# Performance work log

Measured on AMD Instinct MI355X. Metric: run time of the kernel, lower is better.

## Reference

```python
import jax, jax.numpy as jnp
import numpy as np

B, S, D, H = 4, 2048, 512, 8
DEPTH = D // H
BAND = 16  # log_thresholds [1,2,4,8,16] union == distance <= 16


def setup_inputs() -> dict:
    key = jax.random.key(0)
    ks = jax.random.split(key, 11)
    sc = 0.02
    return {
        "q": jax.random.normal(ks[0], (B, S, D), jnp.float32),
        "k": jax.random.normal(ks[1], (B, S, D), jnp.float32),
        "v": jax.random.normal(ks[2], (B, S, D), jnp.float32),
        "wq": jax.random.normal(ks[3], (D, D), jnp.float32) * sc,
        "bq": jnp.zeros((D,), jnp.float32),
        "wk": jax.random.normal(ks[4], (D, D), jnp.float32) * sc,
        "bk": jnp.zeros((D,), jnp.float32),
        "wv": jax.random.normal(ks[5], (D, D), jnp.float32) * sc,
        "bv": jnp.zeros((D,), jnp.float32),
        "wo": jax.random.normal(ks[6], (D, D), jnp.float32) * sc,
        "bo": jnp.zeros((D,), jnp.float32),
    }


def _split_heads(x):
    # [B,S,D] -> [B,H,S,depth]
    b, s, _ = x.shape
    return x.reshape(b, s, H, DEPTH).transpose(0, 2, 1, 3)


def reference(q, k, v, wq, bq, wk, bk, wv, bv, wo, bo):
    qh = _split_heads(q @ wq + bq)
    kh = _split_heads(k @ wk + bk)
    vh = _split_heads(v @ wv + bv)
    scale = 1.0 / jnp.sqrt(jnp.float32(DEPTH))
    logits = jnp.einsum("bhqd,bhkd->bhqk", qh, kh) * scale  # [B,H,S,S]
    idx = jnp.arange(S)
    keep = jnp.abs(idx[:, None] - idx[None, :]) <= BAND  # band mask [S,S]
    logits = jnp.where(keep[None, None], logits, jnp.float32(-1e9))
    attn = jax.nn.softmax(logits, axis=-1)
    out = jnp.einsum("bhqk,bhkd->bhqd", attn, vh)
    out = out.transpose(0, 2, 1, 3).reshape(q.shape[0], -1, D)
    return out @ wo + bo
```

## Files before the change

### kernel.cpp

```cpp
#include <hip/hip_runtime.h>

typedef unsigned int uint;
typedef unsigned short ushort;
typedef __attribute__((ext_vector_type(8))) short bf16x8;
typedef __attribute__((ext_vector_type(4))) float f32x4;

namespace {
constexpr int kS = 2048;
constexpr int kD = 512;
constexpr int kH = 8;
constexpr int kBand = 16;

template <bool C, typename A, typename B> struct cond { using type = A; };
template <typename A, typename B> struct cond<false, A, B> { using type = B; };
}

static __device__ __forceinline__ ushort f2bf(float f) {
  uint u = __builtin_bit_cast(uint, f);
  u = (u + 0x7fffu + ((u >> 16) & 1u)) >> 16;
  return (ushort)u;
}

static __device__ __forceinline__ bf16x8 cvt8(f32x4 lo, f32x4 hi) {
  uint4 r;
  asm("v_cvt_pk_bf16_f32 %0, %1, %2" : "=v"(r.x) : "v"(lo[0]), "v"(lo[1]));
  asm("v_cvt_pk_bf16_f32 %0, %1, %2" : "=v"(r.y) : "v"(lo[2]), "v"(lo[3]));
  asm("v_cvt_pk_bf16_f32 %0, %1, %2" : "=v"(r.z) : "v"(hi[0]), "v"(hi[1]));
  asm("v_cvt_pk_bf16_f32 %0, %1, %2" : "=v"(r.w) : "v"(hi[2]), "v"(hi[3]));
  return __builtin_bit_cast(bf16x8, r);
}

#define GLD16(gp, lp)                                                   \
  __builtin_amdgcn_global_load_lds(                                     \
      (const __attribute__((address_space(1))) uint*)(gp),              \
      (__attribute__((address_space(3))) uint*)(lp), 16, 0, 0)

__global__ __launch_bounds__(256) void prep_kernel(
    const float* __restrict__ wq, const float* __restrict__ wk,
    const float* __restrict__ wv, const float* __restrict__ wo,
    ushort* __restrict__ WT) {
  __shared__ float Ws[64][65];
  const int w = blockIdx.x;
  const int tid = threadIdx.x;
  const int z = w >> 6;
  const float* W = z == 0 ? wq : (z == 1 ? wk : (z == 2 ? wv : wo));
  ushort* T = WT + (size_t)z * kD * kD;
  const int kt = ((w >> 3) & 7) * 64, nt = (w & 7) * 64;
  const int r = tid >> 2, c0 = (tid & 3) * 16;
#pragma unroll
  for (int i = 0; i < 4; ++i) {
    const float4 x =
        *(const float4*)(W + (size_t)(kt + r) * kD + nt + c0 + i * 4);
    Ws[r][c0 + i * 4 + 0] = x.x;
    Ws[r][c0 + i * 4 + 1] = x.y;
    Ws[r][c0 + i * 4 + 2] = x.z;
    Ws[r][c0 + i * 4 + 3] = x.w;
  }
  __syncthreads();
  const int n = tid >> 2, k0 = (tid & 3) * 16;
  alignas(16) ushort tmp[16];
#pragma unroll
  for (int i = 0; i < 16; ++i) tmp[i] = f2bf(Ws[k0 + i][n]);
  ushort* dst = T + (size_t)(nt + n) * kD + kt + k0;
  *(uint4*)(dst + 0) = *(const uint4*)&tmp[0];
  *(uint4*)(dst + 8) = *(const uint4*)&tmp[8];
}

template <int TM, bool AF32>
__global__ __launch_bounds__(256) void gemm_kernel(
    const float* __restrict__ qf, const float* __restrict__ kf,
    const float* __restrict__ vf, const ushort* __restrict__ obp,
    const ushort* __restrict__ WT, const float* __restrict__ bq,
    const float* __restrict__ bk, const float* __restrict__ bv,
    const float* __restrict__ bo, ushort* __restrict__ Qp,
    ushort* __restrict__ Kp, ushort* __restrict__ VT,
    float* __restrict__ outp, int mode_arg) {
  const int mode = mode_arg + blockIdx.z;
  const void* Abv;
  const float* bias;
  switch (mode) {
    case 0: Abv = qf; bias = bq; break;
    case 1: Abv = kf; bias = bk; break;
    case 2: Abv = vf; bias = bv; break;
    default: Abv = obp; bias = bo; break;
  }
  using AT = typename cond<AF32, float, ushort>::type;
  const AT* Abt = (const AT*)Abv;
  const ushort* BT = WT + (size_t)mode * kD * kD;

  constexpr int A_STAGE = TM * (AF32 ? 64 : 32);
  constexpr int B_BASE = 3 * A_STAGE;
  constexpr int NI = (TM == 128) ? 4 : 2;
  constexpr int AI = AF32 ? TM / 32 : TM / 64;
  __shared__ alignas(16) ushort smem[B_BASE + 12288];

  const int tid = threadIdx.x;
  const int wave = tid >> 6, lane = tid & 63, l15 = lane & 15, qd = lane >> 4;
  const int wm = (TM == 128) ? (wave >> 1) * 64 : 0;
  const int wn = (TM == 128) ? (wave & 1) * 64 : wave * 32;
  const int lin = blockIdx.x;
  const int xcd = lin & 7, j = lin >> 3;
  const int rblk = xcd + 8 * (j >> 2), cblk = j & 3;
  const int row0 = rblk * TM, col0 = cblk * 128;
  const int sw = (l15 & 3) ^ (l15 >> 2);

  const AT* pA[AI];
  const ushort* pB[2];
  uint ldsA[AI], ldsB[2];
#pragma unroll
  for (int i = 0; i < AI; ++i) {
    const int linear = i * 256 + tid;
    int r, g;
    if constexpr (AF32) {
      r = linear >> 3;
      g = (linear & 7) ^ (r & 7);
    } else {
      r = linear >> 2;
      g = (linear & 3) ^ ((r & 3) ^ ((r >> 2) & 3));
    }
    pA[i] = Abt + (size_t)(row0 + r) * kD + g * (AF32 ? 4 : 8);
    ldsA[i] = (uint)(i * 256 + wave * 64) * 8;
  }
#pragma unroll
  for (int i = 0; i < 2; ++i) {
    const int linear = i * 256 + tid;
    const int r = linear >> 2, c = linear & 3;
    const int g = c ^ ((r & 3) ^ ((r >> 2) & 3));
    pB[i] = BT + (size_t)(col0 + r) * kD + g * 8;
    ldsB[i] = (uint)B_BASE + (uint)(i * 256 + wave * 64) * 8;
  }

#define ISSUE(kk, st)                                                     \
  {                                                                       \
    _Pragma("unroll") for (int i = 0; i < AI; ++i)                        \
        GLD16(pA[i] + (kk), &smem[ldsA[i] + (st) * A_STAGE]);             \
    _Pragma("unroll") for (int i = 0; i < 2; ++i)                         \
        GLD16(pB[i] + (kk), &smem[ldsB[i] + (st) * 4096]);                \
  }

  f32x4 acc[4][NI];
#pragma unroll
  for (int mi = 0; mi < 4; ++mi)
#pragma unroll
    for (int ni = 0; ni < NI; ++ni) acc[mi][ni] = (f32x4)(0.f);

  ISSUE(0, 0);
  ISSUE(32, 1);
#pragma unroll
  for (int it = 0; it < 16; ++it) {
    if (it < 15) {
      if constexpr (AI + 2 == 6) {
        asm volatile("s_waitcnt vmcnt(6) lgkmcnt(0)\n\ts_barrier" ::: "memory");
      } else {
        static_assert(AI + 2 == 3 || AI + 2 == 6, "unexpected stage size");
        asm volatile("s_waitcnt vmcnt(3) lgkmcnt(0)\n\ts_barrier" ::: "memory");
      }
    } else {
      asm volatile("s_waitcnt vmcnt(0) lgkmcnt(0)\n\ts_barrier" ::: "memory");
    }
    if (it < 14) ISSUE((it + 2) * 32, (it + 2) % 3);
    bf16x8 af[4], br[NI];
    if constexpr (AF32) {
      const float* as = (const float*)&smem[(it % 3) * A_STAGE];
#pragma unroll
      for (int mi = 0; mi < 4; ++mi) {
        const int row = wm + mi * 16 + l15;
        const int s2 = l15 & 7;
        const f32x4 lo = *(const f32x4*)&as[row * 32 + ((2 * qd) ^ s2) * 4];
        const f32x4 hi = *(const f32x4*)&as[row * 32 + ((2 * qd + 1) ^ s2) * 4];
        af[mi] = cvt8(lo, hi);
      }
    } else {
      const ushort* as = &smem[(it % 3) * A_STAGE];
#pragma unroll
      for (int mi = 0; mi < 4; ++mi)
        af[mi] = *(const bf16x8*)&as[(wm + mi * 16 + l15) * 32 + (qd ^ sw) * 8];
    }
    const ushort* bs = &smem[B_BASE + (it % 3) * 4096];
#pragma unroll
    for (int ni = 0; ni < NI; ++ni)
      br[ni] = *(const bf16x8*)&bs[(wn + ni * 16 + l15) * 32 + (qd ^ sw) * 8];
#pragma unroll
    for (int mi = 0; mi < 4; ++mi)
#pragma unroll
      for (int ni = 0; ni < NI; ++ni)
        acc[mi][ni] = __builtin_amdgcn_mfma_f32_16x16x32_bf16(
            af[mi], br[ni], acc[mi][ni], 0, 0, 0);
  }
#undef ISSUE

  float bcol[NI];
#pragma unroll
  for (int ni = 0; ni < NI; ++ni) bcol[ni] = bias[col0 + wn + ni * 16 + l15];

  if (mode == 3) {
#pragma unroll
    for (int mi = 0; mi < 4; ++mi)
#pragma unroll
      for (int ni = 0; ni < NI; ++ni) {
        const int n_g = col0 + wn + ni * 16 + l15;
#pragma unroll
        for (int r = 0; r < 4; ++r) {
          const int token = row0 + wm + mi * 16 + qd * 4 + r;
          outp[(size_t)token * kD + n_g] = acc[mi][ni][r] + bcol[ni];
        }
      }
    return;
  }

  __syncthreads();

  ushort* T = &smem[wave * 4608];
  if (mode <= 1) {
#pragma unroll
    for (int mi = 0; mi < 4; ++mi)
#pragma unroll
      for (int ni = 0; ni < NI; ++ni)
#pragma unroll
        for (int r = 0; r < 4; ++r)
          T[(mi * 16 + qd * 4 + r) * 72 + ni * 16 + l15] =
              f2bf(acc[mi][ni][r] + bcol[ni]);
  } else {
#pragma unroll
    for (int mi = 0; mi < 4; ++mi)
#pragma unroll
      for (int ni = 0; ni < NI; ++ni)
#pragma unroll
        for (int r = 0; r < 4; ++r)
          T[(ni * 16 + l15) * 72 + mi * 16 + qd * 4 + r] =
              f2bf(acc[mi][ni][r] + bcol[ni]);
  }
  asm volatile("s_waitcnt lgkmcnt(0)" ::: "memory");

  const ushort* Trow = &smem[wave * 4608 + lane * 72];
  if (mode <= 1) {
    ushort* C = (mode == 0) ? Qp : Kp;
    ushort* dst = C + (size_t)(row0 + wm + lane) * kD + col0 + wn;
#pragma unroll
    for (int c = 0; c < 8; ++c)
      *(uint4*)(dst + c * 8) = *(const uint4*)(Trow + c * 8);
  } else {
    const int n_g = col0 + wn + lane;
    const int h = n_g >> 6, d = n_g & 63;
    const int t0 = row0 + wm;
    const int b = t0 >> 11, ss = t0 & (kS - 1);
    ushort* dst = VT + ((size_t)(b * kH + h) * 64 + d) * kS + ss;
#pragma unroll
    for (int c = 0; c < 8; ++c)
      *(uint4*)(dst + c * 8) = *(const uint4*)(Trow + c * 8);
  }
}

__global__ __launch_bounds__(64, 1) void attn_kernel(
    const ushort* __restrict__ Qp, const ushort* __restrict__ Kp,
    const ushort* __restrict__ VT, ushort* __restrict__ Ob) {
  __shared__ alignas(16) ushort Pl[64 * 104];

  const int lane = threadIdx.x, l15 = lane & 15, qd = lane >> 4;
  const int bh = blockIdx.y, b = bh >> 3, h = bh & 7;
  const int q0 = blockIdx.x * 64;
  const int colA = h * 64;

  bf16x8 qf[4][2], kf[6][2];
#pragma unroll
  for (int mi = 0; mi < 4; ++mi) {
    const size_t base =
        ((size_t)b * kS + q0 + mi * 16 + l15) * kD + colA + qd * 8;
#pragma unroll
    for (int kc = 0; kc < 2; ++kc)
      qf[mi][kc] = *(const bf16x8*)&Qp[base + kc * 32];
  }
#pragma unroll
  for (int ni = 0; ni < 6; ++ni) {
    int key = q0 - kBand + ni * 16 + l15;
    key = key < 0 ? 0 : (key > kS - 1 ? kS - 1 : key);
    const size_t base = ((size_t)b * kS + key) * kD + colA + qd * 8;
#pragma unroll
    for (int kc = 0; kc < 2; ++kc)
      kf[ni][kc] = *(const bf16x8*)&Kp[base + kc * 32];
  }

  f32x4 S[4][6];
#pragma unroll
  for (int mi = 0; mi < 4; ++mi)
#pragma unroll
    for (int ni = 0; ni < 6; ++ni) S[mi][ni] = (f32x4)(0.f);
#pragma unroll
  for (int mi = 0; mi < 4; ++mi)
#pragma unroll
    for (int ni = 0; ni < 6; ++ni)
#pragma unroll
      for (int kc = 0; kc < 2; ++kc)
        S[mi][ni] = __builtin_amdgcn_mfma_f32_16x16x32_bf16(
            qf[mi][kc], kf[ni][kc], S[mi][ni], 0, 0, 0);

#pragma unroll
  for (int mi = 0; mi < 4; ++mi)
#pragma unroll
    for (int ni = 0; ni < 6; ++ni)
#pragma unroll
      for (int r = 0; r < 4; ++r) {
        const int q_local = mi * 16 + qd * 4 + r;
        const int key_local = ni * 16 + l15;
        const int key = q0 - kBand + key_local;
        const int dlt = key_local - q_local;
        const bool ok = (dlt >= 0) && (dlt <= 32) && (key >= 0) && (key < kS);
        S[mi][ni][r] = ok ? S[mi][ni][r] * 0.125f : -3.0e38f;
      }

  float inv[4][4];
#pragma unroll
  for (int mi = 0; mi < 4; ++mi)
#pragma unroll
    for (int r = 0; r < 4; ++r) {
      float m = S[mi][0][r];
#pragma unroll
      for (int ni = 1; ni < 6; ++ni) m = fmaxf(m, S[mi][ni][r]);
      m = fmaxf(m, __shfl_xor(m, 1));
      m = fmaxf(m, __shfl_xor(m, 2));
      m = fmaxf(m, __shfl_xor(m, 4));
      m = fmaxf(m, __shfl_xor(m, 8));
      float s = 0.f;
#pragma unroll
      for (int ni = 0; ni < 6; ++ni) {
        const float e = __expf(S[mi][ni][r] - m);
        S[mi][ni][r] = e;
        s += e;
      }
      s += __shfl_xor(s, 1);
      s += __shfl_xor(s, 2);
      s += __shfl_xor(s, 4);
      s += __shfl_xor(s, 8);
      inv[mi][r] = 1.f / s;
    }

#pragma unroll
  for (int mi = 0; mi < 4; ++mi)
#pragma unroll
    for (int ni = 0; ni < 6; ++ni)
#pragma unroll
      for (int r = 0; r < 4; ++r)
        Pl[(mi * 16 + qd * 4 + r) * 104 + ni * 16 + l15] = f2bf(S[mi][ni][r]);
  __syncthreads();

  f32x4 O[4][4];
#pragma unroll
  for (int mi = 0; mi < 4; ++mi)
#pragma unroll
    for (int nt = 0; nt < 4; ++nt) O[mi][nt] = (f32x4)(0.f);

#pragma unroll
  for (int kc = 0; kc < 3; ++kc) {
    bf16x8 pf[4], vfr[4];
#pragma unroll
    for (int mi = 0; mi < 4; ++mi)
      pf[mi] = *(const bf16x8*)&Pl[(mi * 16 + l15) * 104 + kc * 32 + qd * 8];
    int kb0 = q0 - kBand + kc * 32 + qd * 8;
    kb0 = kb0 < 0 ? 0 : (kb0 > kS - 8 ? kS - 8 : kb0);
#pragma unroll
    for (int nt = 0; nt < 4; ++nt)
      vfr[nt] =
          *(const bf16x8*)&VT[((size_t)bh * 64 + nt * 16 + l15) * kS + kb0];
#pragma unroll
    for (int mi = 0; mi < 4; ++mi)
#pragma unroll
      for (int nt = 0; nt < 4; ++nt)
        O[mi][nt] = __builtin_amdgcn_mfma_f32_16x16x32_bf16(pf[mi], vfr[nt],
                                                            O[mi][nt], 0, 0, 0);
  }

#pragma unroll
  for (int mi = 0; mi < 4; ++mi)
#pragma unroll
    for (int nt = 0; nt < 4; ++nt)
#pragma unroll
      for (int r = 0; r < 4; ++r)
        Pl[(mi * 16 + qd * 4 + r) * 72 + nt * 16 + l15] =
            f2bf(O[mi][nt][r] * inv[mi][r]);
  asm volatile("s_waitcnt lgkmcnt(0)" ::: "memory");

  ushort* dst = Ob + ((size_t)b * kS + q0 + lane) * kD + colA;
  const ushort* Trow = &Pl[lane * 72];
#pragma unroll
  for (int c = 0; c < 8; ++c)
    *(uint4*)(dst + c * 8) = *(const uint4*)(Trow + c * 8);
}

extern "C" void kernel_launch(void* const* d_in, const int* in_sizes, int n_in,
                              void* d_out, int out_size, void* d_ws,
                              size_t ws_size, hipStream_t stream) {
  const float* q = (const float*)d_in[0];
  const float* k = (const float*)d_in[1];
  const float* v = (const float*)d_in[2];
  const float* wq = (const float*)d_in[3];
  const float* bq = (const float*)d_in[4];
  const float* wk = (const float*)d_in[5];
  const float* bk = (const float*)d_in[6];
  const float* wv = (const float*)d_in[7];
  const float* bv = (const float*)d_in[8];
  const float* wo = (const float*)d_in[9];
  const float* bo = (const float*)d_in[10];
  float* out = (float*)d_out;

  const size_t n1 = (size_t)8192 * kD;
  ushort* Qp = (ushort*)d_ws;
  ushort* Kp = Qp + n1;
  ushort* VT = Kp + n1;
  ushort* Ob = VT + n1;
  ushort* WT = Ob + n1;

  prep_kernel<<<dim3(256), 256, 0, stream>>>(wq, wk, wv, wo, WT);
  gemm_kernel<128, true><<<dim3(256, 1, 3), 256, 0, stream>>>(
      q, k, v, Ob, WT, bq, bk, bv, bo, Qp, Kp, VT, out, 0);
  attn_kernel<<<dim3(kS / 64, 32), 64, 0, stream>>>(Qp, Kp, VT, Ob);
  gemm_kernel<64, false><<<dim3(512, 1, 1), 256, 0, stream>>>(
      q, k, v, Ob, WT, bq, bk, bv, bo, Qp, Kp, VT, out, 3);
}
```

Baseline: 163.7 us.

## Convert fp32 A to bf16 on load in QKV GEMM, shrink attention tiles

The QKV projection GEMM now loads fp32 activations into registers, converts them to bf16 and writes them to LDS one stage ahead, instead of staging raw fp32 via global_load_lds. This halves A-tile LDS footprint and LDS read traffic and allows three blocks per CU, at the cost of register-staged loads. The attention kernel now processes 32 queries per block instead of 64, with a smaller key window and two blocks per CU, for more parallelism and less wasted band compute. The output projection becomes its own specialized kernel.

Result: no change. 161.6 us (-1.3%).

```diff
diff --git a/kernel.cpp b/kernel.cpp
--- a/kernel.cpp
+++ b/kernel.cpp
@@ -10,9 +10,6 @@
 constexpr int kD = 512;
 constexpr int kH = 8;
 constexpr int kBand = 16;
-
-template <bool C, typename A, typename B> struct cond { using type = A; };
-template <typename A, typename B> struct cond<false, A, B> { using type = B; };
 }
 
 static __device__ __forceinline__ ushort f2bf(float f) {
@@ -34,6 +31,8 @@
   __builtin_amdgcn_global_load_lds(                                     \
       (const __attribute__((address_space(1))) uint*)(gp),              \
       (__attribute__((address_space(3))) uint*)(lp), 16, 0, 0)
+
+#define FENCE asm volatile("" ::: "memory")
 
 __global__ __launch_bounds__(256) void prep_kernel(
     const float* __restrict__ wq, const float* __restrict__ wk,
@@ -66,61 +65,39 @@
   *(uint4*)(dst + 8) = *(const uint4*)&tmp[8];
 }
 
-template <int TM, bool AF32>
-__global__ __launch_bounds__(256) void gemm_kernel(
-    const float* __restrict__ qf, const float* __restrict__ kf,
-    const float* __restrict__ vf, const ushort* __restrict__ obp,
-    const ushort* __restrict__ WT, const float* __restrict__ bq,
-    const float* __restrict__ bk, const float* __restrict__ bv,
-    const float* __restrict__ bo, ushort* __restrict__ Qp,
-    ushort* __restrict__ Kp, ushort* __restrict__ VT,
-    float* __restrict__ outp, int mode_arg) {
-  const int mode = mode_arg + blockIdx.z;
-  const void* Abv;
-  const float* bias;
-  switch (mode) {
-    case 0: Abv = qf; bias = bq; break;
-    case 1: Abv = kf; bias = bk; break;
-    case 2: Abv = vf; bias = bv; break;
-    default: Abv = obp; bias = bo; break;
-  }
-  using AT = typename cond<AF32, float, ushort>::type;
-  const AT* Abt = (const AT*)Abv;
+__global__ __launch_bounds__(256, 3) void gemm_qkv(
+    const float* __restrict__ q, const float* __restrict__ k,
+    const float* __restrict__ v, const ushort* __restrict__ WT,
+    const float* __restrict__ bq, const float* __restrict__ bk,
+    const float* __restrict__ bv, ushort* __restrict__ Qp,
+    ushort* __restrict__ Kp, ushort* __restrict__ VT) {
+  const int mode = blockIdx.z;
+  const float* Ab = mode == 0 ? q : (mode == 1 ? k : v);
+  const float* bias = mode == 0 ? bq : (mode == 1 ? bk : bv);
   const ushort* BT = WT + (size_t)mode * kD * kD;
 
-  constexpr int A_STAGE = TM * (AF32 ? 64 : 32);
+  constexpr int A_STAGE = 128 * 32;
   constexpr int B_BASE = 3 * A_STAGE;
-  constexpr int NI = (TM == 128) ? 4 : 2;
-  constexpr int AI = AF32 ? TM / 32 : TM / 64;
   __shared__ alignas(16) ushort smem[B_BASE + 12288];
 
   const int tid = threadIdx.x;
   const int wave = tid >> 6, lane = tid & 63, l15 = lane & 15, qd = lane >> 4;
-  const int wm = (TM == 128) ? (wave >> 1) * 64 : 0;
-  const int wn = (TM == 128) ? (wave & 1) * 64 : wave * 32;
+  const int wm = (wave >> 1) * 64, wn = (wave & 1) * 64;
   const int lin = blockIdx.x;
   const int xcd = lin & 7, j = lin >> 3;
   const int rblk = xcd + 8 * (j >> 2), cblk = j & 3;
-  const int row0 = rblk * TM, col0 = cblk * 128;
+  const int row0 = rblk * 128, col0 = cblk * 128;
   const int sw = (l15 & 3) ^ (l15 >> 2);
 
-  const AT* pA[AI];
+  const int ar = tid >> 1;
+  const int acp = (tid & 1) * 2;
+  const int as_ = (ar & 3) ^ ((ar >> 2) & 3);
+  const float* pAg = Ab + (size_t)(row0 + ar) * kD + acp * 8;
+  const uint wA0 = (uint)(ar * 32 + ((acp ^ as_) * 8));
+  const uint wA1 = (uint)(ar * 32 + (((acp + 1) ^ as_) * 8));
+
   const ushort* pB[2];
-  uint ldsA[AI], ldsB[2];
-#pragma unroll
-  for (int i = 0; i < AI; ++i) {
-    const int linear = i * 256 + tid;
-    int r, g;
-    if constexpr (AF32) {
-      r = linear >> 3;
-      g = (linear & 7) ^ (r & 7);
-    } else {
-      r = linear >> 2;
-      g = (linear & 3) ^ ((r & 3) ^ ((r >> 2) & 3));
-    }
-    pA[i] = Abt + (size_t)(row0 + r) * kD + g * (AF32 ? 4 : 8);
-    ldsA[i] = (uint)(i * 256 + wave * 64) * 8;
-  }
+  uint ldsB[2];
 #pragma unroll
   for (int i = 0; i < 2; ++i) {
     const int linear = i * 256 + tid;
@@ -130,83 +107,71 @@
     ldsB[i] = (uint)B_BASE + (uint)(i * 256 + wave * 64) * 8;
   }
 
-#define ISSUE(kk, st)                                                     \
-  {                                                                       \
-    _Pragma("unroll") for (int i = 0; i < AI; ++i)                        \
-        GLD16(pA[i] + (kk), &smem[ldsA[i] + (st) * A_STAGE]);             \
-    _Pragma("unroll") for (int i = 0; i < 2; ++i)                         \
-        GLD16(pB[i] + (kk), &smem[ldsB[i] + (st) * 4096]);                \
-  }
-
-  f32x4 acc[4][NI];
+  f32x4 areg[2][4];
+#define LOADA(slot, kk)                                               \
+  { _Pragma("unroll") for (int c = 0; c < 4; ++c)                     \
+      areg[slot][c] = *(const f32x4*)(pAg + (kk) + c * 4); }
+#define WRITEA(st, slot)                                              \
+  {                                                                   \
+    *(bf16x8*)&smem[(st) * A_STAGE + wA0] =                           \
+        cvt8(areg[slot][0], areg[slot][1]);                           \
+    *(bf16x8*)&smem[(st) * A_STAGE + wA1] =                           \
+        cvt8(areg[slot][2], areg[slot][3]);                           \
+  }
+#define ISSUEB(kk, st)                                                \
+  { _Pragma("unroll") for (int i = 0; i < 2; ++i)                     \
+      GLD16(pB[i] + (kk), &smem[ldsB[i] + (st) * 4096]); }
+
+  f32x4 acc[4][4];
 #pragma unroll
   for (int mi = 0; mi < 4; ++mi)
 #pragma unroll
-    for (int ni = 0; ni < NI; ++ni) acc[mi][ni] = (f32x4)(0.f);
-
-  ISSUE(0, 0);
-  ISSUE(32, 1);
+    for (int ni = 0; ni < 4; ++ni) acc[mi][ni] = (f32x4)(0.f);
+
+  LOADA(0, 0);
+  FENCE;
+  ISSUEB(0, 0);
+  FENCE;
+  LOADA(1, 32);
+  FENCE;
+  ISSUEB(32, 1);
+  FENCE;
+  WRITEA(0, 0);
+
 #pragma unroll
   for (int it = 0; it < 16; ++it) {
     if (it < 15) {
-      if constexpr (AI + 2 == 6) {
-        asm volatile("s_waitcnt vmcnt(6) lgkmcnt(0)\n\ts_barrier" ::: "memory");
-      } else {
-        static_assert(AI + 2 == 3 || AI + 2 == 6, "unexpected stage size");
-        asm volatile("s_waitcnt vmcnt(3) lgkmcnt(0)\n\ts_barrier" ::: "memory");
-      }
+      WRITEA((it + 1) % 3, (it + 1) & 1);
+      if (it < 14) LOADA(it & 1, (it + 2) * 32);
+      asm volatile("s_waitcnt lgkmcnt(0)\n\ts_barrier" ::: "memory");
+      if (it < 14) ISSUEB((it + 2) * 32, (it + 2) % 3);
+      FENCE;
     } else {
       asm volatile("s_waitcnt vmcnt(0) lgkmcnt(0)\n\ts_barrier" ::: "memory");
     }
-    if (it < 14) ISSUE((it + 2) * 32, (it + 2) % 3);
-    bf16x8 af[4], br[NI];
-    if constexpr (AF32) {
-      const float* as = (const float*)&smem[(it % 3) * A_STAGE];
-#pragma unroll
-      for (int mi = 0; mi < 4; ++mi) {
-        const int row = wm + mi * 16 + l15;
-        const int s2 = l15 & 7;
-        const f32x4 lo = *(const f32x4*)&as[row * 32 + ((2 * qd) ^ s2) * 4];
-        const f32x4 hi = *(const f32x4*)&as[row * 32 + ((2 * qd + 1) ^ s2) * 4];
-        af[mi] = cvt8(lo, hi);
-      }
-    } else {
-      const ushort* as = &smem[(it % 3) * A_STAGE];
-#pragma unroll
-      for (int mi = 0; mi < 4; ++mi)
-        af[mi] = *(const bf16x8*)&as[(wm + mi * 16 + l15) * 32 + (qd ^ sw) * 8];
-    }
+    const ushort* as2 = &smem[(it % 3) * A_STAGE];
     const ushort* bs = &smem[B_BASE + (it % 3) * 4096];
-#pragma unroll
-    for (int ni = 0; ni < NI; ++ni)
+    bf16x8 af[4], br[4];
+#pragma unroll
+    for (int mi = 0; mi < 4; ++mi)
+      af[mi] = *(const bf16x8*)&as2[(wm + mi * 16 + l15) * 32 + (qd ^ sw) * 8];
+#pragma unroll
+    for (int ni = 0; ni < 4; ++ni)
       br[ni] = *(const bf16x8*)&bs[(wn + ni * 16 + l15) * 32 + (qd ^ sw) * 8];
 #pragma unroll
     for (int mi = 0; mi < 4; ++mi)
 #pragma unroll
-      for (int ni = 0; ni < NI; ++ni)
+      for (int ni = 0; ni < 4; ++ni)
         acc[mi][ni] = __builtin_amdgcn_mfma_f32_16x16x32_bf16(
             af[mi], br[ni], acc[mi][ni], 0, 0, 0);
   }
-#undef ISSUE
-
-  float bcol[NI];
-#pragma unroll
-  for (int ni = 0; ni < NI; ++ni) bcol[ni] = bias[col0 + wn + ni * 16 + l15];
-
-  if (mode == 3) {
-#pragma unroll
-    for (int mi = 0; mi < 4; ++mi)
-#pragma unroll
-      for (int ni = 0; ni < NI; ++ni) {
-        const int n_g = col0 + wn + ni * 16 + l15;
-#pragma unroll
-        for (int r = 0; r < 4; ++r) {
-          const int token = row0 + wm + mi * 16 + qd * 4 + r;
-          outp[(size_t)token * kD + n_g] = acc[mi][ni][r] + bcol[ni];
-        }
-      }
-    return;
-  }
+#undef LOADA
+#undef WRITEA
+#undef ISSUEB
+
+  float bcol[4];
+#pragma unroll
+  for (int ni = 0; ni < 4; ++ni) bcol[ni] = bias[col0 + wn + ni * 16 + l15];
 
   __syncthreads();
 
@@ -215,7 +180,7 @@
 #pragma unroll
     for (int mi = 0; mi < 4; ++mi)
 #pragma unroll
-      for (int ni = 0; ni < NI; ++ni)
+      for (int ni = 0; ni < 4; ++ni)
 #pragma unroll
         for (int r = 0; r < 4; ++r)
           T[(mi * 16 + qd * 4 + r) * 72 + ni * 16 + l15] =
@@ -224,7 +189,7 @@
 #pragma unroll
     for (int mi = 0; mi < 4; ++mi)
 #pragma unroll
-      for (int ni = 0; ni < NI; ++ni)
+      for (int ni = 0; ni < 4; ++ni)
 #pragma unroll
         for (int r = 0; r < 4; ++r)
           T[(ni * 16 + l15) * 72 + mi * 16 + qd * 4 + r] =
@@ -251,19 +216,19 @@
   }
 }
 
-__global__ __launch_bounds__(64, 1) void attn_kernel(
+__global__ __launch_bounds__(64, 2) void attn_kernel(
     const ushort* __restrict__ Qp, const ushort* __restrict__ Kp,
     const ushort* __restrict__ VT, ushort* __restrict__ Ob) {
-  __shared__ alignas(16) ushort Pl[64 * 104];
+  __shared__ alignas(16) ushort Pl[32 * 72];
 
   const int lane = threadIdx.x, l15 = lane & 15, qd = lane >> 4;
   const int bh = blockIdx.y, b = bh >> 3, h = bh & 7;
-  const int q0 = blockIdx.x * 64;
+  const int q0 = blockIdx.x * 32;
   const int colA = h * 64;
 
-  bf16x8 qf[4][2], kf[6][2];
-#pragma unroll
-  for (int mi = 0; mi < 4; ++mi) {
+  bf16x8 qf[2][2], kf[4][2];
+#pragma unroll
+  for (int mi = 0; mi < 2; ++mi) {
     const size_t base =
         ((size_t)b * kS + q0 + mi * 16 + l15) * kD + colA + qd * 8;
 #pragma unroll
@@ -271,7 +236,7 @@
       qf[mi][kc] = *(const bf16x8*)&Qp[base + kc * 32];
   }
 #pragma unroll
-  for (int ni = 0; ni < 6; ++ni) {
+  for (int ni = 0; ni < 4; ++ni) {
     int key = q0 - kBand + ni * 16 + l15;
     key = key < 0 ? 0 : (key > kS - 1 ? kS - 1 : key);
     const size_t base = ((size_t)b * kS + key) * kD + colA + qd * 8;
@@ -280,24 +245,24 @@
       kf[ni][kc] = *(const bf16x8*)&Kp[base + kc * 32];
   }
 
-  f32x4 S[4][6];
-#pragma unroll
-  for (int mi = 0; mi < 4; ++mi)
-#pragma unroll
-    for (int ni = 0; ni < 6; ++ni) S[mi][ni] = (f32x4)(0.f);
-#pragma unroll
-  for (int mi = 0; mi < 4; ++mi)
-#pragma unroll
-    for (int ni = 0; ni < 6; ++ni)
+  f32x4 S[2][4];
+#pragma unroll
+  for (int mi = 0; mi < 2; ++mi)
+#pragma unroll
+    for (int ni = 0; ni < 4; ++ni) S[mi][ni] = (f32x4)(0.f);
+#pragma unroll
+  for (int mi = 0; mi < 2; ++mi)
+#pragma unroll
+    for (int ni = 0; ni < 4; ++ni)
 #pragma unroll
       for (int kc = 0; kc < 2; ++kc)
         S[mi][ni] = __builtin_amdgcn_mfma_f32_16x16x32_bf16(
             qf[mi][kc], kf[ni][kc], S[mi][ni], 0, 0, 0);
 
 #pragma unroll
-  for (int mi = 0; mi < 4; ++mi)
-#pragma unroll
-    for (int ni = 0; ni < 6; ++ni)
+  for (int mi = 0; mi < 2; ++mi)
+#pragma unroll
+    for (int ni = 0; ni < 4; ++ni)
 #pragma unroll
       for (int r = 0; r < 4; ++r) {
         const int q_local = mi * 16 + qd * 4 + r;
@@ -308,21 +273,21 @@
         S[mi][ni][r] = ok ? S[mi][ni][r] * 0.125f : -3.0e38f;
       }
 
-  float inv[4][4];
-#pragma unroll
-  for (int mi = 0; mi < 4; ++mi)
+  float inv[2][4];
+#pragma unroll
+  for (int mi = 0; mi < 2; ++mi)
 #pragma unroll
     for (int r = 0; r < 4; ++r) {
       float m = S[mi][0][r];
 #pragma unroll
-      for (int ni = 1; ni < 6; ++ni) m = fmaxf(m, S[mi][ni][r]);
+      for (int ni = 1; ni < 4; ++ni) m = fmaxf(m, S[mi][ni][r]);
       m = fmaxf(m, __shfl_xor(m, 1));
       m = fmaxf(m, __shfl_xor(m, 2));
       m = fmaxf(m, __shfl_xor(m, 4));
       m = fmaxf(m, __shfl_xor(m, 8));
       float s = 0.f;
 #pragma unroll
-      for (int ni = 0; ni < 6; ++ni) {
+      for (int ni = 0; ni < 4; ++ni) {
         const float e = __expf(S[mi][ni][r] - m);
         S[mi][ni][r] = e;
         s += e;
@@ -335,26 +300,26 @@
     }
 
 #pragma unroll
-  for (int mi = 0; mi < 4; ++mi)
-#pragma unroll
-    for (int ni = 0; ni < 6; ++ni)
+  for (int mi = 0; mi < 2; ++mi)
+#pragma unroll
+    for (int ni = 0; ni < 4; ++ni)
 #pragma unroll
       for (int r = 0; r < 4; ++r)
-        Pl[(mi * 16 + qd * 4 + r) * 104 + ni * 16 + l15] = f2bf(S[mi][ni][r]);
+        Pl[(mi * 16 + qd * 4 + r) * 72 + ni * 16 + l15] = f2bf(S[mi][ni][r]);
   __syncthreads();
 
-  f32x4 O[4][4];
-#pragma unroll
-  for (int mi = 0; mi < 4; ++mi)
+  f32x4 O[2][4];
+#pragma unroll
+  for (int mi = 0; mi < 2; ++mi)
 #pragma unroll
     for (int nt = 0; nt < 4; ++nt) O[mi][nt] = (f32x4)(0.f);
 
 #pragma unroll
-  for (int kc = 0; kc < 3; ++kc) {
-    bf16x8 pf[4], vfr[4];
-#pragma unroll
-    for (int mi = 0; mi < 4; ++mi)
-      pf[mi] = *(const bf16x8*)&Pl[(mi * 16 + l15) * 104 + kc * 32 + qd * 8];
+  for (int kc = 0; kc < 2; ++kc) {
+    bf16x8 pf[2], vfr[4];
+#pragma unroll
+    for (int mi = 0; mi < 2; ++mi)
+      pf[mi] = *(const bf16x8*)&Pl[(mi * 16 + l15) * 72 + kc * 32 + qd * 8];
     int kb0 = q0 - kBand + kc * 32 + qd * 8;
     kb0 = kb0 < 0 ? 0 : (kb0 > kS - 8 ? kS - 8 : kb0);
 #pragma unroll
@@ -362,7 +327,7 @@
       vfr[nt] =
           *(const bf16x8*)&VT[((size_t)bh * 64 + nt * 16 + l15) * kS + kb0];
 #pragma unroll
-    for (int mi = 0; mi < 4; ++mi)
+    for (int mi = 0; mi < 2; ++mi)
 #pragma unroll
       for (int nt = 0; nt < 4; ++nt)
         O[mi][nt] = __builtin_amdgcn_mfma_f32_16x16x32_bf16(pf[mi], vfr[nt],
@@ -370,7 +335,7 @@
   }
 
 #pragma unroll
-  for (int mi = 0; mi < 4; ++mi)
+  for (int mi = 0; mi < 2; ++mi)
 #pragma unroll
     for (int nt = 0; nt < 4; ++nt)
 #pragma unroll
@@ -379,11 +344,101 @@
             f2bf(O[mi][nt][r] * inv[mi][r]);
   asm volatile("s_waitcnt lgkmcnt(0)" ::: "memory");
 
-  ushort* dst = Ob + ((size_t)b * kS + q0 + lane) * kD + colA;
-  const ushort* Trow = &Pl[lane * 72];
-#pragma unroll
-  for (int c = 0; c < 8; ++c)
+  const int row = lane >> 1, half = lane & 1;
+  ushort* dst = Ob + ((size_t)b * kS + q0 + row) * kD + colA + half * 32;
+  const ushort* Trow = &Pl[row * 72 + half * 32];
+#pragma unroll
+  for (int c = 0; c < 4; ++c)
     *(uint4*)(dst + c * 8) = *(const uint4*)(Trow + c * 8);
+}
+
+__global__ __launch_bounds__(256) void gemm_out(
+    const ushort* __restrict__ Ab, const ushort* __restrict__ BT,
+    const float* __restrict__ bias, float* __restrict__ outp) {
+  constexpr int A_STAGE = 64 * 32;
+  constexpr int B_BASE = 3 * A_STAGE;
+  __shared__ alignas(16) ushort smem[B_BASE + 12288];
+
+  const int tid = threadIdx.x;
+  const int wave = tid >> 6, lane = tid & 63, l15 = lane & 15, qd = lane >> 4;
+  const int wn = wave * 32;
+  const int lin = blockIdx.x;
+  const int xcd = lin & 7, j = lin >> 3;
+  const int rblk = xcd + 8 * (j >> 2), cblk = j & 3;
+  const int row0 = rblk * 64, col0 = cblk * 128;
+  const int sw = (l15 & 3) ^ (l15 >> 2);
+
+  const ushort* pA0;
+  uint ldsA0;
+  {
+    const int r = tid >> 2, c = tid & 3;
+    const int g = c ^ ((r & 3) ^ ((r >> 2) & 3));
+    pA0 = Ab + (size_t)(row0 + r) * kD + g * 8;
+    ldsA0 = (uint)(wave * 64) * 8;
+  }
+  const ushort* pB[2];
+  uint ldsB[2];
+#pragma unroll
+  for (int i = 0; i < 2; ++i) {
+    const int linear = i * 256 + tid;
+    const int r = linear >> 2, c = linear & 3;
+    const int g = c ^ ((r & 3) ^ ((r >> 2) & 3));
+    pB[i] = BT + (size_t)(col0 + r) * kD + g * 8;
+    ldsB[i] = (uint)B_BASE + (uint)(i * 256 + wave * 64) * 8;
+  }
+
+#define ISSUE3(kk, st)                                                \
+  {                                                                   \
+    GLD16(pA0 + (kk), &smem[ldsA0 + (st) * A_STAGE]);                 \
+    _Pragma("unroll") for (int i = 0; i < 2; ++i)                     \
+        GLD16(pB[i] + (kk), &smem[ldsB[i] + (st) * 4096]);            \
+  }
+
+  f32x4 acc[4][2];
+#pragma unroll
+  for (int mi = 0; mi < 4; ++mi)
+#pragma unroll
+    for (int ni = 0; ni < 2; ++ni) acc[mi][ni] = (f32x4)(0.f);
+
+  ISSUE3(0, 0);
+  ISSUE3(32, 1);
+#pragma unroll
+  for (int it = 0; it < 16; ++it) {
+    if (it < 15)
+      asm volatile("s_waitcnt vmcnt(3) lgkmcnt(0)\n\ts_barrier" ::: "memory");
+    else
+      asm volatile("s_waitcnt vmcnt(0) lgkmcnt(0)\n\ts_barrier" ::: "memory");
+    if (it < 14) ISSUE3((it + 2) * 32, (it + 2) % 3);
+    const ushort* as2 = &smem[(it % 3) * A_STAGE];
+    const ushort* bs = &smem[B_BASE + (it % 3) * 4096];
+    bf16x8 af[4], br[2];
+#pragma unroll
+    for (int mi = 0; mi < 4; ++mi)
+      af[mi] = *(const bf16x8*)&as2[(mi * 16 + l15) * 32 + (qd ^ sw) * 8];
+#pragma unroll
+    for (int ni = 0; ni < 2; ++ni)
+      br[ni] = *(const bf16x8*)&bs[(wn + ni * 16 + l15) * 32 + (qd ^ sw) * 8];
+#pragma unroll
+    for (int mi = 0; mi < 4; ++mi)
+#pragma unroll
+      for (int ni = 0; ni < 2; ++ni)
+        acc[mi][ni] = __builtin_amdgcn_mfma_f32_16x16x32_bf16(
+            af[mi], br[ni], acc[mi][ni], 0, 0, 0);
+  }
+#undef ISSUE3
+
+#pragma unroll
+  for (int ni = 0; ni < 2; ++ni) {
+    const int n_g = col0 + wn + ni * 16 + l15;
+    const float bc = bias[n_g];
+#pragma unroll
+    for (int mi = 0; mi < 4; ++mi)
+#pragma unroll
+      for (int r = 0; r < 4; ++r) {
+        const int token = row0 + mi * 16 + qd * 4 + r;
+        outp[(size_t)token * kD + n_g] = acc[mi][ni][r] + bc;
+      }
+  }
 }
 
 extern "C" void kernel_launch(void* const* d_in, const int* in_sizes, int n_in,
@@ -410,9 +465,9 @@
   ushort* WT = Ob + n1;
 
   prep_kernel<<<dim3(256), 256, 0, stream>>>(wq, wk, wv, wo, WT);
-  gemm_kernel<128, true><<<dim3(256, 1, 3), 256, 0, stream>>>(
-      q, k, v, Ob, WT, bq, bk, bv, bo, Qp, Kp, VT, out, 0);
-  attn_kernel<<<dim3(kS / 64, 32), 64, 0, stream>>>(Qp, Kp, VT, Ob);
-  gemm_kernel<64, false><<<dim3(512, 1, 1), 256, 0, stream>>>(
-      q, k, v, Ob, WT, bq, bk, bv, bo, Qp, Kp, VT, out, 3);
-}
+  gemm_qkv<<<dim3(256, 1, 3), 256, 0, stream>>>(q, k, v, WT, bq, bk, bv, Qp,
+                                                Kp, VT);
+  attn_kernel<<<dim3(kS / 32, 32), 64, 0, stream>>>(Qp, Kp, VT, Ob);
+  gemm_out<<<dim3(512), 256, 0, stream>>>(Ob, WT + (size_t)3 * kD * kD, bo,
+                                          out);
+}
```
